# Kernel tuning notes

Hardware: AMD Instinct MI355X
Metric: run time of the kernel (lower is better)

Reference implementation:

```python
import jax, jax.numpy as jnp
import numpy as np

N = 25000          # nodes
E = 400000         # edges (before self-loops)
IN_CH = 256
HID = 128
HEADS = 4
OUT_CH = 64
NEG_SLOPE = 0.2    # PyG GATConv default LeakyReLU slope


def setup_inputs() -> dict:
    key = jax.random.key(0)
    ks = jax.random.split(key, 10)
    x = jax.random.normal(ks[0], (N, IN_CH), dtype=jnp.float32)
    edge_index = jax.random.randint(ks[1], (2, E), 0, N, dtype=jnp.int64)
    s = 0.05
    return {
        "x": x,
        "edge_index": edge_index,
        "W1": jax.random.normal(ks[2], (IN_CH, HEADS * HID), dtype=jnp.float32) * s,
        "a_src1": jax.random.normal(ks[3], (HEADS, HID), dtype=jnp.float32) * s,
        "a_dst1": jax.random.normal(ks[4], (HEADS, HID), dtype=jnp.float32) * s,
        "b1": jnp.zeros((HEADS * HID,), dtype=jnp.float32),
        "W2": jax.random.normal(ks[5], (HEADS * HID, OUT_CH), dtype=jnp.float32) * s,
        "a_src2": jax.random.normal(ks[6], (1, OUT_CH), dtype=jnp.float32) * s,
        "a_dst2": jax.random.normal(ks[7], (1, OUT_CH), dtype=jnp.float32) * s,
        "b2": jnp.zeros((OUT_CH,), dtype=jnp.float32),
    }


def gat_layer(x, src, dst, W, a_src, a_dst, b, concat):
    """PyG-style GATConv (self-loops already in src/dst)."""
    H, C = a_src.shape
    h = (x @ W).reshape(-1, H, C)                       # [N, H, C]
    es = jnp.einsum('nhc,hc->nh', h, a_src)             # [N, H]
    ed = jnp.einsum('nhc,hc->nh', h, a_dst)
    e = es[src] + ed[dst]                               # [Etot, H]
    e = jnp.where(e > 0, e, NEG_SLOPE * e)              # LeakyReLU
    # segment softmax over incoming edges per destination node
    m = jax.lax.stop_gradient(jax.ops.segment_max(e, dst, num_segments=N))
    p = jnp.exp(e - m[dst])
    denom = jax.ops.segment_sum(p, dst, num_segments=N)
    alpha = p / (denom[dst] + 1e-16)                    # [Etot, H]
    msg = h[src] * alpha[:, :, None]                    # [Etot, H, C]
    out = jax.ops.segment_sum(msg, dst, num_segments=N)  # [N, H, C]
    out = out.reshape(N, H * C) if concat else out.mean(axis=1)
    return out + b


def reference(x, edge_index, W1, a_src1, a_dst1, b1, W2, a_src2, a_dst2, b2):
    loop = jnp.arange(N, dtype=edge_index.dtype)
    src = jnp.concatenate([edge_index[0], loop])        # add self-loops
    dst = jnp.concatenate([edge_index[1], loop])
    h = gat_layer(x, src, dst, W1, a_src1, a_dst1, b1, concat=True)
    h = jax.nn.elu(h)
    return gat_layer(h, src, dst, W2, a_src2, a_dst2, b2, concat=False)
```

## Files before the change

kernel.cpp:

```cpp
#include <hip/hip_runtime.h>
#include <math.h>

#define N_NODES 25000
#define N_EDGES 400000
#define E_TOT   (N_EDGES + N_NODES)
#define IN_CH   256
#define HID     128
#define HEADS   4
#define OUT_CH  64
#define HC1     512
#define CAP     48
#define PL      (N_NODES * CAP)

static inline int cdiv(int a, int b) { return (a + b - 1) / b; }

typedef __attribute__((ext_vector_type(8))) short bf16x8;
typedef __attribute__((ext_vector_type(4))) float f32x4;
typedef __attribute__((ext_vector_type(2))) float f32x2;
typedef __attribute__((ext_vector_type(4))) unsigned u32x4;

__device__ __forceinline__ unsigned short f2bf(float f) {
  union { float f; unsigned u; } v; v.f = f;
  unsigned r = v.u + 0x7fffu + ((v.u >> 16) & 1u);
  return (unsigned short)(r >> 16);
}
__device__ __forceinline__ float bf2f(unsigned short b) {
  union { unsigned u; float f; } v; v.u = ((unsigned)b) << 16;
  return v.f;
}
__device__ __forceinline__ float lrelu(float v) { return v > 0.f ? v : 0.2f * v; }

__device__ __forceinline__ void glds16(const unsigned short* g, unsigned short* l) {
  __builtin_amdgcn_global_load_lds(
      (const __attribute__((address_space(1))) void*)g,
      (__attribute__((address_space(3))) void*)l, 16, 0, 0);
}

__device__ __forceinline__ void acc_pk(f32x2 (&acc2)[4], u32x4 hd, float p) {
  f32x2 pv = {p, p};
#pragma unroll
  for (int d = 0; d < 4; d++) {
    f32x2 hx;
    hx.x = __uint_as_float(hd[d] << 16);
    hx.y = __uint_as_float(hd[d] & 0xffff0000u);
    acc2[d] = __builtin_elementwise_fma(hx, pv, acc2[d]);
  }
}

template <int K, int H, bool BF>
__device__ __forceinline__ void es_body(int nb, const void* __restrict__ in_,
                                        const float* __restrict__ wboth,
                                        float* __restrict__ es,
                                        float* __restrict__ ed) {
  const int O = 2 * H;
  const int KPL = K / 64;
  int lane = threadIdx.x & 63, wid = threadIdx.x >> 6;
  int n = nb * 4 + wid;
  if (n >= N_NODES) return;
  float wreg[KPL][O];
#pragma unroll
  for (int j = 0; j < KPL; j++)
#pragma unroll
    for (int o = 0; o < O; o++) wreg[j][o] = wboth[(size_t)(lane * KPL + j) * O + o];
  float p[O];
#pragma unroll
  for (int o = 0; o < O; o++) p[o] = 0.f;
  if (BF) {
    bf16x8 v8 = *(const bf16x8*)((const unsigned short*)in_ + (size_t)n * K + lane * KPL);
#pragma unroll
    for (int j = 0; j < KPL; j++) {
      float v = bf2f((unsigned short)v8[j]);
#pragma unroll
      for (int o = 0; o < O; o++) p[o] = fmaf(v, wreg[j][o], p[o]);
    }
  } else {
    float4 v4 = *(const float4*)((const float*)in_ + (size_t)n * K + lane * KPL);
    float vv[4] = {v4.x, v4.y, v4.z, v4.w};
#pragma unroll
    for (int j = 0; j < KPL; j++) {
#pragma unroll
      for (int o = 0; o < O; o++) p[o] = fmaf(vv[j], wreg[j][o], p[o]);
    }
  }
#pragma unroll
  for (int off = 32; off > 0; off >>= 1)
#pragma unroll
    for (int o = 0; o < O; o++) p[o] += __shfl_xor(p[o], off, 64);
  if (lane == 0) {
#pragma unroll
    for (int h = 0; h < H; h++) { es[n * H + h] = p[h]; ed[n * H + h] = p[H + h]; }
  }
}

#define B_FILL 1661
#define B_CAST 6250
#define B_WT1  512
#define B_WT2  128
#define B_F1   8
#define B_F2   4
__global__ __launch_bounds__(256) void prep_k(
    const int* __restrict__ srcs, const int* __restrict__ dsts, int* __restrict__ cnt,
    int* __restrict__ bucket,
    const float* __restrict__ x, unsigned short* __restrict__ xb,
    const float* __restrict__ W1, unsigned short* __restrict__ Wt1,
    const float* __restrict__ W2, unsigned short* __restrict__ Wt2,
    const float* __restrict__ as1, const float* __restrict__ ad1, float* __restrict__ wb1,
    const float* __restrict__ as2, const float* __restrict__ ad2, float* __restrict__ wb2) {
  int b = blockIdx.x, t = threadIdx.x;
  if (b < B_FILL) {
    int e = b * 256 + t;
    if (e < E_TOT) {
      int s, d;
      if (e < N_EDGES) { s = srcs[e]; d = dsts[e]; } else { s = d = e - N_EDGES; }
      int pos = atomicAdd(&cnt[d], 1);
      if (pos < CAP) bucket[d * CAP + pos] = s;
    }
  } else if (b < B_FILL + B_CAST) {
    int i = (b - B_FILL) * 256 + t;
    float4 v = *(const float4*)(x + (size_t)i * 4);
    ushort4 o;
    o.x = f2bf(v.x); o.y = f2bf(v.y); o.z = f2bf(v.z); o.w = f2bf(v.w);
    *(ushort4*)(xb + (size_t)i * 4) = o;
  } else if (b < B_FILL + B_CAST + B_WT1) {
    int i = (b - B_FILL - B_CAST) * 256 + t;
    int n = i / IN_CH, k = i % IN_CH;
    Wt1[i] = f2bf(W1[(size_t)k * HC1 + n]);
  } else if (b < B_FILL + B_CAST + B_WT1 + B_WT2) {
    int i = (b - B_FILL - B_CAST - B_WT1) * 256 + t;
    int n = i / HC1, k = i % HC1;
    Wt2[i] = f2bf(W2[(size_t)k * OUT_CH + n]);
  } else if (b < B_FILL + B_CAST + B_WT1 + B_WT2 + B_F1) {
    int i = (b - B_FILL - B_CAST - B_WT1 - B_WT2) * 256 + t;
    int k = i / 8, o = i % 8;
    int h = (o < 4) ? o : o - 4;
    const float* a = (o < 4) ? as1 : ad1;
    float acc = 0.f;
    for (int c = 0; c < HID; c++)
      acc += W1[(size_t)k * HC1 + h * HID + c] * a[h * HID + c];
    wb1[i] = acc;
  } else {
    int i = (b - B_FILL - B_CAST - B_WT1 - B_WT2 - B_F1) * 256 + t;
    int k = i / 2, o = i % 2;
    const float* a = (o < 1) ? as2 : ad2;
    float acc = 0.f;
    for (int c = 0; c < OUT_CH; c++)
      acc += W2[(size_t)k * OUT_CH + c] * a[c];
    wb2[i] = acc;
  }
}

template <int BN>
__device__ __forceinline__ void gemm_body(
    unsigned short* __restrict__ As, unsigned short* __restrict__ Bs,
    const unsigned short* __restrict__ A, const unsigned short* __restrict__ Bt,
    unsigned short* __restrict__ C, int M, int N, int K, int bx, int by) {
  const int BM = 128, BK = 32;
  const int NB = BN / 32;
  int tid = threadIdx.x;
  int w = tid >> 6, l = tid & 63;
  int wr = w >> 1, wc = w & 1;
  int row0 = by * BM, col0 = bx * BN;
  int lr = l & 15, kg = l >> 4;
  int lrow = l >> 2, lk = (l & 3) * 8;

  f32x4 acc[4][NB] = {};

  int ar0 = min(row0 + w * 16 + lrow, M - 1);
  int ar1 = min(row0 + 64 + w * 16 + lrow, M - 1);
  const unsigned short* Ap0 = A + (size_t)ar0 * K + lk;
  const unsigned short* Ap1 = A + (size_t)ar1 * K + lk;
  unsigned short* AsW0 = As + (w * 16) * BK;
  unsigned short* AsW1 = As + (64 + w * 16) * BK;
  const unsigned short* Bp0 = Bt + (size_t)(col0 + w * 16 + lrow) * K + lk;
  unsigned short* BsW0 = Bs + (w * 16) * BK;
  int bcol1 = (BN == 128) ? (col0 + 64 + w * 16 + lrow) : 0;
  const unsigned short* Bp1 = Bt + (size_t)bcol1 * K + lk;
  unsigned short* BsW1 = Bs + ((BN == 128 ? 64 + w * 16 : 0)) * BK;

  for (int k0 = 0; k0 < K; k0 += BK) {
    glds16(Ap0 + k0, AsW0);
    glds16(Ap1 + k0, AsW1);
    glds16(Bp0 + k0, BsW0);
    if (BN == 128) glds16(Bp1 + k0, BsW1);
    __syncthreads();
    bf16x8 af[4], bfr[NB];
#pragma unroll
    for (int m = 0; m < 4; m++)
      af[m] = *(const bf16x8*)&As[(wr * 64 + m * 16 + lr) * BK + kg * 8];
#pragma unroll
    for (int n = 0; n < NB; n++)
      bfr[n] = *(const bf16x8*)&Bs[(wc * (BN / 2) + n * 16 + lr) * BK + kg * 8];
#pragma unroll
    for (int m = 0; m < 4; m++)
#pragma unroll
      for (int n = 0; n < NB; n++)
        acc[m][n] = __builtin_amdgcn_mfma_f32_16x16x32_bf16(af[m], bfr[n], acc[m][n], 0, 0, 0);
    __syncthreads();
  }
#pragma unroll
  for (int m = 0; m < 4; m++) {
#pragma unroll
    for (int n = 0; n < NB; n++) {
      int col = col0 + wc * (BN / 2) + n * 16 + lr;
#pragma unroll
      for (int r = 0; r < 4; r++) {
        int row = row0 + wr * 64 + m * 16 + kg * 4 + r;
        if (row < M) C[(size_t)row * N + col] = f2bf(acc[m][n][r]);
      }
    }
  }
}

#define G1_BLK 784
#define B_SORT 98
__global__ __launch_bounds__(256) void gemm1_sort_es1_k(
    const unsigned short* __restrict__ xb, const unsigned short* __restrict__ Wt1,
    unsigned short* __restrict__ h1b,
    const int* __restrict__ cnt, int* __restrict__ order,
    const float* __restrict__ wb1,
    float* __restrict__ es1, float* __restrict__ ed1) {
  __shared__ __attribute__((aligned(16))) unsigned short As[128 * 32];
  __shared__ __attribute__((aligned(16))) unsigned short Bs[128 * 32];
  int b = blockIdx.x;
  if (b < G1_BLK) {
    gemm_body<128>(As, Bs, xb, Wt1, h1b, N_NODES, HC1, IN_CH, b & 3, b >> 2);
  } else if (b < G1_BLK + B_SORT) {
    int i = (b - G1_BLK) * 256 + threadIdx.x;
    if (i >= N_NODES) return;
    int w0 = i & ~31;
    int wend = min(w0 + 32, N_NODES);
    int mydeg = cnt[i];
    int rank = 0;
    for (int j = w0; j < wend; j++) {
      int dj = cnt[j];
      rank += (dj < mydeg) || (dj == mydeg && j < i);
    }
    order[w0 + rank] = i;
  } else {
    es_body<IN_CH, HEADS, true>(b - G1_BLK - B_SORT, xb, wb1, es1, ed1);
  }
}

#define G2_BLK 196
__global__ __launch_bounds__(256) void gemm2_es2_k(
    const unsigned short* __restrict__ out1b, const unsigned short* __restrict__ Wt2,
    unsigned short* __restrict__ h2b,
    const float* __restrict__ wb2, float* __restrict__ es2, float* __restrict__ ed2) {
  __shared__ __attribute__((aligned(16))) unsigned short As[128 * 32];
  __shared__ __attribute__((aligned(16))) unsigned short Bs[64 * 32];
  int b = blockIdx.x;
  if (b < G2_BLK) {
    gemm_body<64>(As, Bs, out1b, Wt2, h2b, N_NODES, OUT_CH, HC1, 0, b);
  } else {
    es_body<HC1, 1, true>(b - G2_BLK, out1b, wb2, es2, ed2);
  }
}

__global__ __launch_bounds__(256) void gat_agg1_g8(
    const unsigned short* __restrict__ hfeat,
    const float* __restrict__ es, const float* __restrict__ ed,
    const int* __restrict__ cnt, const int* __restrict__ bucket,
    const int* __restrict__ order,
    const float* __restrict__ bias, unsigned short* __restrict__ out) {
  int b = blockIdx.x;
  int g = b & 7;
  int lane = threadIdx.x & 63, wid = threadIdx.x >> 6;
  int grp = lane >> 3, cl = lane & 7;
  int gi = (b >> 3) * 32 + wid * 8 + grp;
  bool valid = gi < N_NODES;
  int n = order[valid ? gi : 0];
  int h = g >> 1;
  unsigned c0 = (unsigned)(g * 64 + cl * 8);
  int beg = n * CAP;
  int end = beg + min(cnt[n], CAP);
  int gbase = grp * 8;
  float ednh = ed[n * 4 + h];

  f32x2 acc2[4] = {};
  float sum = 0.f;
  for (int i = beg; i < end; i += 8) {
    int idx = i + cl;
    bool inb = idx < end;
    int sv = bucket[inb ? idx : end - 1];
    float av = inb ? __expf(lrelu(es[sv * 4 + h] + ednh)) : 0.f;
    sum += av;
#pragma unroll
    for (int e = 0; e < 8; e++) {
      unsigned s = (unsigned)__shfl(sv, gbase + e, 64);
      float p = __shfl(av, gbase + e, 64);
      u32x4 hv = *(const u32x4*)(hfeat + ((s << 9) + c0));
      acc_pk(acc2, hv, p);
    }
  }
#pragma unroll
  for (int off = 1; off < 8; off <<= 1) sum += __shfl_xor(sum, off, 64);
  if (valid) {
    float inv = 1.f / (sum + 1e-16f);
    bf16x8 o;
#pragma unroll
    for (int d = 0; d < 4; d++) {
      float va = acc2[d].x * inv + bias[c0 + 2 * d];
      float vb = acc2[d].y * inv + bias[c0 + 2 * d + 1];
      va = va > 0.f ? va : expm1f(va);
      vb = vb > 0.f ? vb : expm1f(vb);
      o[2 * d] = (short)f2bf(va);
      o[2 * d + 1] = (short)f2bf(vb);
    }
    *(bf16x8*)(out + (size_t)n * 512 + c0) = o;
  }
}

__global__ __launch_bounds__(256) void gat_agg2_g8(
    const unsigned short* __restrict__ hfeat,
    const float* __restrict__ es, const float* __restrict__ ed,
    const int* __restrict__ cnt, const int* __restrict__ bucket,
    const int* __restrict__ order,
    const float* __restrict__ bias, float* __restrict__ out) {
  int lane = threadIdx.x & 63, wid = threadIdx.x >> 6;
  int grp = lane >> 3, cl = lane & 7;
  int gi = blockIdx.x * 32 + wid * 8 + grp;
  bool valid = gi < N_NODES;
  int n = order[valid ? gi : 0];
  unsigned c0 = (unsigned)(cl * 8);
  int beg = n * CAP;
  int end = beg + min(cnt[n], CAP);
  int gbase = grp * 8;
  float edn = ed[n];

  f32x2 acc2[4] = {};
  float sum = 0.f;
  for (int i = beg; i < end; i += 8) {
    int idx = i + cl;
    bool inb = idx < end;
    int sv = bucket[inb ? idx : end - 1];
    float av = inb ? __expf(lrelu(es[sv] + edn)) : 0.f;
    sum += av;
#pragma unroll
    for (int e = 0; e < 8; e++) {
      unsigned s = (unsigned)__shfl(sv, gbase + e, 64);
      float p = __shfl(av, gbase + e, 64);
      u32x4 hv = *(const u32x4*)(hfeat + ((s << 6) + c0));
      acc_pk(acc2, hv, p);
    }
  }
#pragma unroll
  for (int off = 1; off < 8; off <<= 1) sum += __shfl_xor(sum, off, 64);
  if (valid) {
    float inv = 1.f / (sum + 1e-16f);
    float4 o0, o1;
    o0.x = acc2[0].x * inv + bias[c0];
    o0.y = acc2[0].y * inv + bias[c0 + 1];
    o0.z = acc2[1].x * inv + bias[c0 + 2];
    o0.w = acc2[1].y * inv + bias[c0 + 3];
    o1.x = acc2[2].x * inv + bias[c0 + 4];
    o1.y = acc2[2].y * inv + bias[c0 + 5];
    o1.z = acc2[3].x * inv + bias[c0 + 6];
    o1.w = acc2[3].y * inv + bias[c0 + 7];
    *(float4*)(out + (size_t)n * 64 + c0) = o0;
    *(float4*)(out + (size_t)n * 64 + c0 + 4) = o1;
  }
}

extern "C" void kernel_launch(void* const* d_in, const int* in_sizes, int n_in,
                              void* d_out, int out_size, void* d_ws, size_t ws_size,
                              hipStream_t stream) {
  const float* x   = (const float*)d_in[0];
  const int*   ei  = (const int*)d_in[1];
  const float* W1  = (const float*)d_in[2];
  const float* as1 = (const float*)d_in[3];
  const float* ad1 = (const float*)d_in[4];
  const float* b1  = (const float*)d_in[5];
  const float* W2  = (const float*)d_in[6];
  const float* as2 = (const float*)d_in[7];
  const float* ad2 = (const float*)d_in[8];
  const float* b2  = (const float*)d_in[9];
  float* out = (float*)d_out;

  const int* srcs = ei;
  const int* dsts = ei + N_EDGES;

  char* ws = (char*)d_ws;
  auto alloc = [&](size_t bytes) -> char* {
    char* p = ws;
    ws += (bytes + 255) & ~(size_t)255;
    return p;
  };
  unsigned short* xb    = (unsigned short*)alloc((size_t)N_NODES * IN_CH * 2);
  unsigned short* Wt1   = (unsigned short*)alloc((size_t)IN_CH * HC1 * 2);
  unsigned short* Wt2   = (unsigned short*)alloc((size_t)HC1 * OUT_CH * 2);
  unsigned short* h1b   = (unsigned short*)alloc((size_t)N_NODES * HC1 * 2);
  unsigned short* out1b = (unsigned short*)alloc((size_t)N_NODES * HC1 * 2);
  unsigned short* h2b   = (unsigned short*)alloc((size_t)N_NODES * OUT_CH * 2);
  float* wb1    = (float*)alloc((size_t)IN_CH * 2 * HEADS * 4);
  float* wb2    = (float*)alloc((size_t)HC1 * 2 * 4);
  float* es1    = (float*)alloc((size_t)N_NODES * HEADS * 4);
  float* ed1    = (float*)alloc((size_t)N_NODES * HEADS * 4);
  float* es2    = (float*)alloc((size_t)N_NODES * 4);
  float* ed2    = (float*)alloc((size_t)N_NODES * 4);
  int*   cnt    = (int*)alloc((size_t)N_NODES * 4);
  int*   bucket = (int*)alloc((size_t)PL * 4);
  int*   order  = (int*)alloc((size_t)N_NODES * 4);

  hipMemsetAsync(cnt, 0, (size_t)N_NODES * 4, stream);

  const int gn4 = cdiv(N_NODES, 4);
  const int gn32 = cdiv(N_NODES, 32);

  prep_k<<<B_FILL + B_CAST + B_WT1 + B_WT2 + B_F1 + B_F2, 256, 0, stream>>>(
      srcs, dsts, cnt, bucket, x, xb, W1, Wt1, W2, Wt2,
      as1, ad1, wb1, as2, ad2, wb2);
  gemm1_sort_es1_k<<<G1_BLK + B_SORT + gn4, 256, 0, stream>>>(
      xb, Wt1, h1b, cnt, order, wb1, es1, ed1);
  gat_agg1_g8<<<gn32 * 8, 256, 0, stream>>>(
      h1b, es1, ed1, cnt, bucket, order, b1, out1b);
  gemm2_es2_k<<<G2_BLK + gn4, 256, 0, stream>>>(
      out1b, Wt2, h2b, wb2, es2, ed2);
  gat_agg2_g8<<<gn32, 256, 0, stream>>>(h2b, es2, ed2, cnt, bucket, order, b2, out);
}
```

Before: 164.7 us.

## Merge five kernels into one cooperative persistent kernel with grid syncs

Replaces the five separate launches (prep, gemm1/sort/es1, agg1, gemm2/es2, agg2) with a single cooperative kernel. Each phase runs as a grid-stride loop over its old block indices, with grid.sync between phases. The aim is to remove kernel launch gaps and pipeline drain between stages. In exchange, grid-wide barriers are added, and occupancy is limited to the residency the merged kernel allows. Registers go to the max across phases, and the __restrict__ qualifiers are dropped.

Result: slower. 401.7 us (+143.9%).

```diff
diff --git a/kernel.cpp b/kernel.cpp
--- a/kernel.cpp
+++ b/kernel.cpp
@@ -1,5 +1,8 @@
 #include <hip/hip_runtime.h>
+#include <hip/hip_cooperative_groups.h>
 #include <math.h>
+
+namespace cg = cooperative_groups;
 
 #define N_NODES 25000
 #define N_EDGES 400000
@@ -47,11 +50,20 @@
   }
 }
 
+struct Params {
+  const int* srcs; const int* dsts;
+  const float* x;
+  const float* W1; const float* as1; const float* ad1; const float* b1;
+  const float* W2; const float* as2; const float* ad2; const float* b2;
+  float* out;
+  unsigned short *xb, *Wt1, *Wt2, *h1b, *out1b, *h2b;
+  float *wb1, *wb2, *es1, *ed1, *es2, *ed2;
+  int *cnt, *bucket, *order;
+};
+
 template <int K, int H, bool BF>
-__device__ __forceinline__ void es_body(int nb, const void* __restrict__ in_,
-                                        const float* __restrict__ wboth,
-                                        float* __restrict__ es,
-                                        float* __restrict__ ed) {
+__device__ __forceinline__ void es_body(int nb, const void* in_,
+                                        const float* wboth, float* es, float* ed) {
   const int O = 2 * H;
   const int KPL = K / 64;
   int lane = threadIdx.x & 63, wid = threadIdx.x >> 6;
@@ -92,68 +104,11 @@
   }
 }
 
-#define B_FILL 1661
-#define B_CAST 6250
-#define B_WT1  512
-#define B_WT2  128
-#define B_F1   8
-#define B_F2   4
-__global__ __launch_bounds__(256) void prep_k(
-    const int* __restrict__ srcs, const int* __restrict__ dsts, int* __restrict__ cnt,
-    int* __restrict__ bucket,
-    const float* __restrict__ x, unsigned short* __restrict__ xb,
-    const float* __restrict__ W1, unsigned short* __restrict__ Wt1,
-    const float* __restrict__ W2, unsigned short* __restrict__ Wt2,
-    const float* __restrict__ as1, const float* __restrict__ ad1, float* __restrict__ wb1,
-    const float* __restrict__ as2, const float* __restrict__ ad2, float* __restrict__ wb2) {
-  int b = blockIdx.x, t = threadIdx.x;
-  if (b < B_FILL) {
-    int e = b * 256 + t;
-    if (e < E_TOT) {
-      int s, d;
-      if (e < N_EDGES) { s = srcs[e]; d = dsts[e]; } else { s = d = e - N_EDGES; }
-      int pos = atomicAdd(&cnt[d], 1);
-      if (pos < CAP) bucket[d * CAP + pos] = s;
-    }
-  } else if (b < B_FILL + B_CAST) {
-    int i = (b - B_FILL) * 256 + t;
-    float4 v = *(const float4*)(x + (size_t)i * 4);
-    ushort4 o;
-    o.x = f2bf(v.x); o.y = f2bf(v.y); o.z = f2bf(v.z); o.w = f2bf(v.w);
-    *(ushort4*)(xb + (size_t)i * 4) = o;
-  } else if (b < B_FILL + B_CAST + B_WT1) {
-    int i = (b - B_FILL - B_CAST) * 256 + t;
-    int n = i / IN_CH, k = i % IN_CH;
-    Wt1[i] = f2bf(W1[(size_t)k * HC1 + n]);
-  } else if (b < B_FILL + B_CAST + B_WT1 + B_WT2) {
-    int i = (b - B_FILL - B_CAST - B_WT1) * 256 + t;
-    int n = i / HC1, k = i % HC1;
-    Wt2[i] = f2bf(W2[(size_t)k * OUT_CH + n]);
-  } else if (b < B_FILL + B_CAST + B_WT1 + B_WT2 + B_F1) {
-    int i = (b - B_FILL - B_CAST - B_WT1 - B_WT2) * 256 + t;
-    int k = i / 8, o = i % 8;
-    int h = (o < 4) ? o : o - 4;
-    const float* a = (o < 4) ? as1 : ad1;
-    float acc = 0.f;
-    for (int c = 0; c < HID; c++)
-      acc += W1[(size_t)k * HC1 + h * HID + c] * a[h * HID + c];
-    wb1[i] = acc;
-  } else {
-    int i = (b - B_FILL - B_CAST - B_WT1 - B_WT2 - B_F1) * 256 + t;
-    int k = i / 2, o = i % 2;
-    const float* a = (o < 1) ? as2 : ad2;
-    float acc = 0.f;
-    for (int c = 0; c < OUT_CH; c++)
-      acc += W2[(size_t)k * OUT_CH + c] * a[c];
-    wb2[i] = acc;
-  }
-}
-
 template <int BN>
 __device__ __forceinline__ void gemm_body(
-    unsigned short* __restrict__ As, unsigned short* __restrict__ Bs,
-    const unsigned short* __restrict__ A, const unsigned short* __restrict__ Bt,
-    unsigned short* __restrict__ C, int M, int N, int K, int bx, int by) {
+    unsigned short* As, unsigned short* Bs,
+    const unsigned short* A, const unsigned short* Bt,
+    unsigned short* C, int M, int N, int K, int bx, int by) {
   const int BM = 128, BK = 32;
   const int NB = BN / 32;
   int tid = threadIdx.x;
@@ -211,84 +166,111 @@
   }
 }
 
+#define B_FILL 1661
+#define B_CAST 6250
+#define B_WT1  512
+#define B_WT2  128
+#define B_F1   8
+#define B_F2   4
+#define A_BLOCKS (B_FILL + B_CAST + B_WT1 + B_WT2 + B_F1 + B_F2)
+__device__ __forceinline__ void prep_body(int b, const Params& P) {
+  int t = threadIdx.x;
+  if (b < B_FILL) {
+    int e = b * 256 + t;
+    if (e < E_TOT) {
+      int s, d;
+      if (e < N_EDGES) { s = P.srcs[e]; d = P.dsts[e]; } else { s = d = e - N_EDGES; }
+      int pos = atomicAdd(&P.cnt[d], 1);
+      if (pos < CAP) P.bucket[d * CAP + pos] = s;
+    }
+  } else if (b < B_FILL + B_CAST) {
+    int i = (b - B_FILL) * 256 + t;
+    float4 v = *(const float4*)(P.x + (size_t)i * 4);
+    ushort4 o;
+    o.x = f2bf(v.x); o.y = f2bf(v.y); o.z = f2bf(v.z); o.w = f2bf(v.w);
+    *(ushort4*)(P.xb + (size_t)i * 4) = o;
+  } else if (b < B_FILL + B_CAST + B_WT1) {
+    int i = (b - B_FILL - B_CAST) * 256 + t;
+    int n = i / IN_CH, k = i % IN_CH;
+    P.Wt1[i] = f2bf(P.W1[(size_t)k * HC1 + n]);
+  } else if (b < B_FILL + B_CAST + B_WT1 + B_WT2) {
+    int i = (b - B_FILL - B_CAST - B_WT1) * 256 + t;
+    int n = i / HC1, k = i % HC1;
+    P.Wt2[i] = f2bf(P.W2[(size_t)k * OUT_CH + n]);
+  } else if (b < B_FILL + B_CAST + B_WT1 + B_WT2 + B_F1) {
+    int i = (b - B_FILL - B_CAST - B_WT1 - B_WT2) * 256 + t;
+    int k = i / 8, o = i % 8;
+    int h = (o < 4) ? o : o - 4;
+    const float* a = (o < 4) ? P.as1 : P.ad1;
+    float acc = 0.f;
+    for (int c = 0; c < HID; c++)
+      acc += P.W1[(size_t)k * HC1 + h * HID + c] * a[h * HID + c];
+    P.wb1[i] = acc;
+  } else {
+    int i = (b - B_FILL - B_CAST - B_WT1 - B_WT2 - B_F1) * 256 + t;
+    int k = i / 2, o = i % 2;
+    const float* a = (o < 1) ? P.as2 : P.ad2;
+    float acc = 0.f;
+    for (int c = 0; c < OUT_CH; c++)
+      acc += P.W2[(size_t)k * OUT_CH + c] * a[c];
+    P.wb2[i] = acc;
+  }
+}
+
 #define G1_BLK 784
 #define B_SORT 98
-__global__ __launch_bounds__(256) void gemm1_sort_es1_k(
-    const unsigned short* __restrict__ xb, const unsigned short* __restrict__ Wt1,
-    unsigned short* __restrict__ h1b,
-    const int* __restrict__ cnt, int* __restrict__ order,
-    const float* __restrict__ wb1,
-    float* __restrict__ es1, float* __restrict__ ed1) {
-  __shared__ __attribute__((aligned(16))) unsigned short As[128 * 32];
-  __shared__ __attribute__((aligned(16))) unsigned short Bs[128 * 32];
-  int b = blockIdx.x;
+#define GN4    6250
+#define PB_BLOCKS (G1_BLK + B_SORT + GN4)
+__device__ __forceinline__ void phaseB_body(int b, const Params& P,
+                                            unsigned short* As, unsigned short* Bs) {
   if (b < G1_BLK) {
-    gemm_body<128>(As, Bs, xb, Wt1, h1b, N_NODES, HC1, IN_CH, b & 3, b >> 2);
+    gemm_body<128>(As, Bs, P.xb, P.Wt1, P.h1b, N_NODES, HC1, IN_CH, b & 3, b >> 2);
   } else if (b < G1_BLK + B_SORT) {
     int i = (b - G1_BLK) * 256 + threadIdx.x;
     if (i >= N_NODES) return;
     int w0 = i & ~31;
     int wend = min(w0 + 32, N_NODES);
-    int mydeg = cnt[i];
+    int mydeg = P.cnt[i];
     int rank = 0;
     for (int j = w0; j < wend; j++) {
-      int dj = cnt[j];
+      int dj = P.cnt[j];
       rank += (dj < mydeg) || (dj == mydeg && j < i);
     }
-    order[w0 + rank] = i;
+    P.order[w0 + rank] = i;
   } else {
-    es_body<IN_CH, HEADS, true>(b - G1_BLK - B_SORT, xb, wb1, es1, ed1);
-  }
-}
-
-#define G2_BLK 196
-__global__ __launch_bounds__(256) void gemm2_es2_k(
-    const unsigned short* __restrict__ out1b, const unsigned short* __restrict__ Wt2,
-    unsigned short* __restrict__ h2b,
-    const float* __restrict__ wb2, float* __restrict__ es2, float* __restrict__ ed2) {
-  __shared__ __attribute__((aligned(16))) unsigned short As[128 * 32];
-  __shared__ __attribute__((aligned(16))) unsigned short Bs[64 * 32];
-  int b = blockIdx.x;
-  if (b < G2_BLK) {
-    gemm_body<64>(As, Bs, out1b, Wt2, h2b, N_NODES, OUT_CH, HC1, 0, b);
-  } else {
-    es_body<HC1, 1, true>(b - G2_BLK, out1b, wb2, es2, ed2);
-  }
-}
-
-__global__ __launch_bounds__(256) void gat_agg1_g8(
-    const unsigned short* __restrict__ hfeat,
-    const float* __restrict__ es, const float* __restrict__ ed,
-    const int* __restrict__ cnt, const int* __restrict__ bucket,
-    const int* __restrict__ order,
-    const float* __restrict__ bias, unsigned short* __restrict__ out) {
-  int b = blockIdx.x;
+    es_body<IN_CH, HEADS, true>(b - G1_BLK - B_SORT, P.xb, P.wb1, P.es1, P.ed1);
+  }
+}
+
+#define GN32 782
+#define PC_BLOCKS (GN32 * 8)
+__device__ __forceinline__ void agg1_body(int b, const Params& P) {
   int g = b & 7;
   int lane = threadIdx.x & 63, wid = threadIdx.x >> 6;
   int grp = lane >> 3, cl = lane & 7;
   int gi = (b >> 3) * 32 + wid * 8 + grp;
   bool valid = gi < N_NODES;
-  int n = order[valid ? gi : 0];
+  int n = P.order[valid ? gi : 0];
   int h = g >> 1;
   unsigned c0 = (unsigned)(g * 64 + cl * 8);
   int beg = n * CAP;
-  int end = beg + min(cnt[n], CAP);
+  int end = beg + min(P.cnt[n], CAP);
   int gbase = grp * 8;
-  float ednh = ed[n * 4 + h];
+  float ednh = P.ed1[n * 4 + h];
 
   f32x2 acc2[4] = {};
   float sum = 0.f;
   for (int i = beg; i < end; i += 8) {
     int idx = i + cl;
     bool inb = idx < end;
-    int sv = bucket[inb ? idx : end - 1];
-    float av = inb ? __expf(lrelu(es[sv * 4 + h] + ednh)) : 0.f;
+    int sv = P.bucket[inb ? idx : end - 1];
+    float av = inb ? __expf(lrelu(P.es1[sv * 4 + h] + ednh)) : 0.f;
     sum += av;
 #pragma unroll
     for (int e = 0; e < 8; e++) {
       unsigned s = (unsigned)__shfl(sv, gbase + e, 64);
       float p = __shfl(av, gbase + e, 64);
-      u32x4 hv = *(const u32x4*)(hfeat + ((s << 9) + c0));
+      u32x4 hv = *(const u32x4*)(P.h1b + ((s << 9) + c0));
       acc_pk(acc2, hv, p);
     }
   }
@@ -299,47 +281,54 @@
     bf16x8 o;
 #pragma unroll
     for (int d = 0; d < 4; d++) {
-      float va = acc2[d].x * inv + bias[c0 + 2 * d];
-      float vb = acc2[d].y * inv + bias[c0 + 2 * d + 1];
+      float va = acc2[d].x * inv + P.b1[c0 + 2 * d];
+      float vb = acc2[d].y * inv + P.b1[c0 + 2 * d + 1];
       va = va > 0.f ? va : expm1f(va);
       vb = vb > 0.f ? vb : expm1f(vb);
       o[2 * d] = (short)f2bf(va);
       o[2 * d + 1] = (short)f2bf(vb);
     }
-    *(bf16x8*)(out + (size_t)n * 512 + c0) = o;
-  }
-}
-
-__global__ __launch_bounds__(256) void gat_agg2_g8(
-    const unsigned short* __restrict__ hfeat,
-    const float* __restrict__ es, const float* __restrict__ ed,
-    const int* __restrict__ cnt, const int* __restrict__ bucket,
-    const int* __restrict__ order,
-    const float* __restrict__ bias, float* __restrict__ out) {
+    *(bf16x8*)(P.out1b + (size_t)n * 512 + c0) = o;
+  }
+}
+
+#define G2_BLK 196
+#define PD_BLOCKS (G2_BLK + GN4)
+__device__ __forceinline__ void phaseD_body(int b, const Params& P,
+                                            unsigned short* As, unsigned short* Bs) {
+  if (b < G2_BLK) {
+    gemm_body<64>(As, Bs, P.out1b, P.Wt2, P.h2b, N_NODES, OUT_CH, HC1, 0, b);
+  } else {
+    es_body<HC1, 1, true>(b - G2_BLK, P.out1b, P.wb2, P.es2, P.ed2);
+  }
+}
+
+#define PE_BLOCKS GN32
+__device__ __forceinline__ void agg2_body(int b, const Params& P) {
   int lane = threadIdx.x & 63, wid = threadIdx.x >> 6;
   int grp = lane >> 3, cl = lane & 7;
-  int gi = blockIdx.x * 32 + wid * 8 + grp;
+  int gi = b * 32 + wid * 8 + grp;
   bool valid = gi < N_NODES;
-  int n = order[valid ? gi : 0];
+  int n = P.order[valid ? gi : 0];
   unsigned c0 = (unsigned)(cl * 8);
   int beg = n * CAP;
-  int end = beg + min(cnt[n], CAP);
+  int end = beg + min(P.cnt[n], CAP);
   int gbase = grp * 8;
-  float edn = ed[n];
+  float edn = P.ed2[n];
 
   f32x2 acc2[4] = {};
   float sum = 0.f;
   for (int i = beg; i < end; i += 8) {
     int idx = i + cl;
     bool inb = idx < end;
-    int sv = bucket[inb ? idx : end - 1];
-    float av = inb ? __expf(lrelu(es[sv] + edn)) : 0.f;
+    int sv = P.bucket[inb ? idx : end - 1];
+    float av = inb ? __expf(lrelu(P.es2[sv] + edn)) : 0.f;
     sum += av;
 #pragma unroll
     for (int e = 0; e < 8; e++) {
       unsigned s = (unsigned)__shfl(sv, gbase + e, 64);
       float p = __shfl(av, gbase + e, 64);
-      u32x4 hv = *(const u32x4*)(hfeat + ((s << 6) + c0));
+      u32x4 hv = *(const u32x4*)(P.h2b + ((s << 6) + c0));
       acc_pk(acc2, hv, p);
     }
   }
@@ -348,36 +337,52 @@
   if (valid) {
     float inv = 1.f / (sum + 1e-16f);
     float4 o0, o1;
-    o0.x = acc2[0].x * inv + bias[c0];
-    o0.y = acc2[0].y * inv + bias[c0 + 1];
-    o0.z = acc2[1].x * inv + bias[c0 + 2];
-    o0.w = acc2[1].y * inv + bias[c0 + 3];
-    o1.x = acc2[2].x * inv + bias[c0 + 4];
-    o1.y = acc2[2].y * inv + bias[c0 + 5];
-    o1.z = acc2[3].x * inv + bias[c0 + 6];
-    o1.w = acc2[3].y * inv + bias[c0 + 7];
-    *(float4*)(out + (size_t)n * 64 + c0) = o0;
-    *(float4*)(out + (size_t)n * 64 + c0 + 4) = o1;
-  }
+    o0.x = acc2[0].x * inv + P.b2[c0];
+    o0.y = acc2[0].y * inv + P.b2[c0 + 1];
+    o0.z = acc2[1].x * inv + P.b2[c0 + 2];
+    o0.w = acc2[1].y * inv + P.b2[c0 + 3];
+    o1.x = acc2[2].x * inv + P.b2[c0 + 4];
+    o1.y = acc2[2].y * inv + P.b2[c0 + 5];
+    o1.z = acc2[3].x * inv + P.b2[c0 + 6];
+    o1.w = acc2[3].y * inv + P.b2[c0 + 7];
+    *(float4*)(P.out + (size_t)n * 64 + c0) = o0;
+    *(float4*)(P.out + (size_t)n * 64 + c0 + 4) = o1;
+  }
+}
+
+__global__ __launch_bounds__(256) void mega_k(Params P) {
+  cg::grid_group grid = cg::this_grid();
+  __shared__ __attribute__((aligned(16))) unsigned short As[128 * 32];
+  __shared__ __attribute__((aligned(16))) unsigned short Bs[128 * 32];
+
+  for (int b = blockIdx.x; b < A_BLOCKS; b += gridDim.x) prep_body(b, P);
+  grid.sync();
+  for (int b = blockIdx.x; b < PB_BLOCKS; b += gridDim.x) phaseB_body(b, P, As, Bs);
+  grid.sync();
+  for (int b = blockIdx.x; b < PC_BLOCKS; b += gridDim.x) agg1_body(b, P);
+  grid.sync();
+  for (int b = blockIdx.x; b < PD_BLOCKS; b += gridDim.x) phaseD_body(b, P, As, Bs);
+  grid.sync();
+  for (int b = blockIdx.x; b < PE_BLOCKS; b += gridDim.x) agg2_body(b, P);
 }
 
 extern "C" void kernel_launch(void* const* d_in, const int* in_sizes, int n_in,
                               void* d_out, int out_size, void* d_ws, size_t ws_size,
                               hipStream_t stream) {
-  const float* x   = (const float*)d_in[0];
-  const int*   ei  = (const int*)d_in[1];
-  const float* W1  = (const float*)d_in[2];
-  const float* as1 = (const float*)d_in[3];
-  const float* ad1 = (const float*)d_in[4];
-  const float* b1  = (const float*)d_in[5];
-  const float* W2  = (const float*)d_in[6];
-  const float* as2 = (const float*)d_in[7];
-  const float* ad2 = (const float*)d_in[8];
-  const float* b2  = (const float*)d_in[9];
-  float* out = (float*)d_out;
-
-  const int* srcs = ei;
-  const int* dsts = ei + N_EDGES;
+  Params P;
+  P.x   = (const float*)d_in[0];
+  const int* ei = (const int*)d_in[1];
+  P.W1  = (const float*)d_in[2];
+  P.as1 = (const float*)d_in[3];
+  P.ad1 = (const float*)d_in[4];
+  P.b1  = (const float*)d_in[5];
+  P.W2  = (const float*)d_in[6];
+  P.as2 = (const float*)d_in[7];
+  P.ad2 = (const float*)d_in[8];
+  P.b2  = (const float*)d_in[9];
+  P.out = (float*)d_out;
+  P.srcs = ei;
+  P.dsts = ei + N_EDGES;
 
   char* ws = (char*)d_ws;
   auto alloc = [&](size_t bytes) -> char* {
@@ -385,35 +390,35 @@
     ws += (bytes + 255) & ~(size_t)255;
     return p;
   };
-  unsigned short* xb    = (unsigned short*)alloc((size_t)N_NODES * IN_CH * 2);
-  unsigned short* Wt1   = (unsigned short*)alloc((size_t)IN_CH * HC1 * 2);
-  unsigned short* Wt2   = (unsigned short*)alloc((size_t)HC1 * OUT_CH * 2);
-  unsigned short* h1b   = (unsigned short*)alloc((size_t)N_NODES * HC1 * 2);
-  unsigned short* out1b = (unsigned short*)alloc((size_t)N_NODES * HC1 * 2);
-  unsigned short* h2b   = (unsigned short*)alloc((size_t)N_NODES * OUT_CH * 2);
-  float* wb1    = (float*)alloc((size_t)IN_CH * 2 * HEADS * 4);
-  float* wb2    = (float*)alloc((size_t)HC1 * 2 * 4);
-  float* es1    = (float*)alloc((size_t)N_NODES * HEADS * 4);
-  float* ed1    = (float*)alloc((size_t)N_NODES * HEADS * 4);
-  float* es2    = (float*)alloc((size_t)N_NODES * 4);
-  float* ed2    = (float*)alloc((size_t)N_NODES * 4);
-  int*   cnt    = (int*)alloc((size_t)N_NODES * 4);
-  int*   bucket = (int*)alloc((size_t)PL * 4);
-  int*   order  = (int*)alloc((size_t)N_NODES * 4);
-
-  hipMemsetAsync(cnt, 0, (size_t)N_NODES * 4, stream);
-
-  const int gn4 = cdiv(N_NODES, 4);
-  const int gn32 = cdiv(N_NODES, 32);
-
-  prep_k<<<B_FILL + B_CAST + B_WT1 + B_WT2 + B_F1 + B_F2, 256, 0, stream>>>(
-      srcs, dsts, cnt, bucket, x, xb, W1, Wt1, W2, Wt2,
-      as1, ad1, wb1, as2, ad2, wb2);
-  gemm1_sort_es1_k<<<G1_BLK + B_SORT + gn4, 256, 0, stream>>>(
-      xb, Wt1, h1b, cnt, order, wb1, es1, ed1);
-  gat_agg1_g8<<<gn32 * 8, 256, 0, stream>>>(
-      h1b, es1, ed1, cnt, bucket, order, b1, out1b);
-  gemm2_es2_k<<<G2_BLK + gn4, 256, 0, stream>>>(
-      out1b, Wt2, h2b, wb2, es2, ed2);
-  gat_agg2_g8<<<gn32, 256, 0, stream>>>(h2b, es2, ed2, cnt, bucket, order, b2, out);
-}
+  P.xb    = (unsigned short*)alloc((size_t)N_NODES * IN_CH * 2);
+  P.Wt1   = (unsigned short*)alloc((size_t)IN_CH * HC1 * 2);
+  P.Wt2   = (unsigned short*)alloc((size_t)HC1 * OUT_CH * 2);
+  P.h1b   = (unsigned short*)alloc((size_t)N_NODES * HC1 * 2);
+  P.out1b = (unsigned short*)alloc((size_t)N_NODES * HC1 * 2);
+  P.h2b   = (unsigned short*)alloc((size_t)N_NODES * OUT_CH * 2);
+  P.wb1   = (float*)alloc((size_t)IN_CH * 2 * HEADS * 4);
+  P.wb2   = (float*)alloc((size_t)HC1 * 2 * 4);
+  P.es1   = (float*)alloc((size_t)N_NODES * HEADS * 4);
+  P.ed1   = (float*)alloc((size_t)N_NODES * HEADS * 4);
+  P.es2   = (float*)alloc((size_t)N_NODES * 4);
+  P.ed2   = (float*)alloc((size_t)N_NODES * 4);
+  P.cnt   = (int*)alloc((size_t)N_NODES * 4);
+  P.bucket= (int*)alloc((size_t)PL * 4);
+  P.order = (int*)alloc((size_t)N_NODES * 4);
+
+  hipMemsetAsync(P.cnt, 0, (size_t)N_NODES * 4, stream);
+
+  int nbPerCU = 0;
+  hipOccupancyMaxActiveBlocksPerMultiprocessor(&nbPerCU, (const void*)mega_k, 256, 0);
+  if (nbPerCU < 1) nbPerCU = 1;
+  int numCU = 0;
+  hipDeviceGetAttribute(&numCU, hipDeviceAttributeMultiprocessorCount, 0);
+  if (numCU < 1) numCU = 256;
+  long long grid = (long long)nbPerCU * numCU;
+  if (grid > PC_BLOCKS + 2048) grid = PC_BLOCKS + 2048;
+
+  Params* pArg = &P;
+  void* args[] = {(void*)pArg};
+  hipLaunchCooperativeKernel((const void*)mega_k, dim3((unsigned)grid), dim3(256),
+                             args, 0, stream);
+}
```
